# Kernel optimization log

Measured on AMD Instinct MI355X. Metric: run time of the kernel, lower is better.

Reference implementation:

```python
import jax, jax.numpy as jnp
import numpy as np

D_MODEL = 1024
HEADS = 16
D_K = D_MODEL // HEADS


def setup_inputs() -> dict:
    key = jax.random.key(0)
    ks = jax.random.split(key, 11)
    bs, seq = 2, 2048
    scale = 1.0 / np.sqrt(D_MODEL)
    inp = {
        "query": jax.random.normal(ks[0], (bs, seq, D_MODEL), jnp.float32),
        "key": jax.random.normal(ks[1], (bs, seq, D_MODEL), jnp.float32),
        "value": jax.random.normal(ks[2], (bs, seq, D_MODEL), jnp.float32),
        # nn.Linear weights: y = x @ W.T + b, W shape [out, in]
        "Wq": jax.random.normal(ks[3], (D_MODEL, D_MODEL), jnp.float32) * scale,
        "bq": jnp.zeros((D_MODEL,), jnp.float32),
        "Wk": jax.random.normal(ks[4], (D_MODEL, D_MODEL), jnp.float32) * scale,
        "bk": jnp.zeros((D_MODEL,), jnp.float32),
        "Wv": jax.random.normal(ks[5], (D_MODEL, D_MODEL), jnp.float32) * scale,
        "bv": jnp.zeros((D_MODEL,), jnp.float32),
        "Wo": jax.random.normal(ks[6], (D_MODEL, D_MODEL), jnp.float32) * scale,
        "bo": jnp.zeros((D_MODEL,), jnp.float32),
    }
    return inp


def _split_heads(x, bs):
    # [b, s, d_model] -> [b, h, s, d_k]
    return x.reshape(bs, -1, HEADS, D_K).transpose(0, 2, 1, 3)


def reference(query, key, value, Wq, bq, Wk, bk, Wv, bv, Wo, bo):
    bs = query.shape[0]
    q = _split_heads(query @ Wq.T + bq, bs)
    k = _split_heads(key @ Wk.T + bk, bs)
    v = _split_heads(value @ Wv.T + bv, bs)
    # scaled dot-product attention (dropout is identity at eval)
    logits = jnp.einsum("bhqd,bhkd->bhqk", q, k) / np.sqrt(D_K).astype(np.float32)
    probs = jax.nn.softmax(logits, axis=-1)
    scores = jnp.einsum("bhqk,bhkd->bhqd", probs, v)  # [b, h, s, d_k]
    concat = scores.transpose(0, 2, 1, 3).reshape(bs, -1, D_MODEL)
    output = concat @ Wo.T + bo
    return (output, scores)
```

## Files before the change

### kernel.cpp

```cpp
#include <hip/hip_runtime.h>
#include <stdint.h>
#include <math.h>

typedef __bf16 bf16;
typedef __bf16 bf16x4 __attribute__((ext_vector_type(4)));
typedef __bf16 bf16x8 __attribute__((ext_vector_type(8)));
typedef float floatx4 __attribute__((ext_vector_type(4)));
typedef float floatx16 __attribute__((ext_vector_type(16)));

#define CEXP 0.1803368801111204f

__global__ __launch_bounds__(256) void wcvt_kernel(
    const float* __restrict__ Wq, const float* __restrict__ Wk,
    const float* __restrict__ Wv, const float* __restrict__ Wo,
    bf16* __restrict__ dst)
{
  const float* src = (blockIdx.y == 0) ? Wq : (blockIdx.y == 1) ? Wk
                   : (blockIdx.y == 2) ? Wv : Wo;
  bf16* d = dst + (size_t)blockIdx.y * 1048576;
  const int i = (blockIdx.x * 256 + threadIdx.x) * 4;
  const floatx4 v = *(const floatx4*)(src + i);
  bf16x4 o;
#pragma unroll
  for (int j = 0; j < 4; ++j) o[j] = (bf16)v[j];
  *(bf16x4*)(d + i) = o;
}

__device__ __forceinline__ void gemm_body(
    const float* __restrict__ A, const bf16* __restrict__ Ab,
    const bf16* __restrict__ Wb, const float* __restrict__ bias,
    void* __restrict__ Cout, const int mode, const float oscale)
{
  __shared__ __align__(16) bf16 As[128 * 72];
  __shared__ __align__(16) bf16 Bs[128 * 72];
  const int tid  = threadIdx.x;
  const int wave = tid >> 6;
  const int lane = tid & 63;
  const int mlane = lane & 15;
  const int quad  = lane >> 4;
  const int m0 = blockIdx.x * 128;
  const int n0 = blockIdx.y * 128;
  const int wm = (wave >> 1) * 64;
  const int wn = (wave & 1) * 64;
  const int arow = tid >> 4, ac4 = (tid & 15) * 4;
  const int wrow = tid >> 3, wc8 = (tid & 7) * 8;

  floatx4 a_pf[8];
  bf16x8  ab_pf[4];
  bf16x8  w_pf[4];

  auto load_a = [&](int k0) {
    if (mode == 1) {
#pragma unroll
      for (int c = 0; c < 4; ++c) {
        const int token = m0 + c * 32 + wrow;
        const int b = token >> 11, s = token & 2047;
        const int h = k0 >> 6;
        ab_pf[c] = *(const bf16x8*)(Ab + (((size_t)(b * 16 + h) * 2048 + s) << 6) + wc8);
      }
    } else {
#pragma unroll
      for (int rr = 0; rr < 8; ++rr)
        a_pf[rr] = *(const floatx4*)(A + (size_t)(m0 + rr * 16 + arow) * 1024 + k0 + ac4);
    }
  };
  auto load_w = [&](int k0) {
#pragma unroll
    for (int c = 0; c < 4; ++c)
      w_pf[c] = *(const bf16x8*)(Wb + (size_t)(n0 + c * 32 + wrow) * 1024 + k0 + wc8);
  };

  load_a(0);
  load_w(0);

  floatx4 acc[4][4] = {};

  for (int k0 = 0; k0 < 1024; k0 += 64) {
    if (mode == 1) {
#pragma unroll
      for (int c = 0; c < 4; ++c)
        *(bf16x8*)&As[(c * 32 + wrow) * 72 + wc8] = ab_pf[c];
    } else {
#pragma unroll
      for (int rr = 0; rr < 8; ++rr) {
        bf16x4 ac;
#pragma unroll
        for (int j = 0; j < 4; ++j) ac[j] = (bf16)a_pf[rr][j];
        *(bf16x4*)&As[(rr * 16 + arow) * 72 + ac4] = ac;
      }
    }
#pragma unroll
    for (int c = 0; c < 4; ++c)
      *(bf16x8*)&Bs[(c * 32 + wrow) * 72 + wc8] = w_pf[c];
    __syncthreads();

    if (k0 + 64 < 1024) { load_a(k0 + 64); load_w(k0 + 64); }

#pragma unroll
    for (int kk = 0; kk < 64; kk += 32) {
      bf16x8 af[4], bfr[4];
#pragma unroll
      for (int t = 0; t < 4; ++t) {
        af[t]  = *(const bf16x8*)&As[(wm + t * 16 + mlane) * 72 + kk + quad * 8];
        bfr[t] = *(const bf16x8*)&Bs[(wn + t * 16 + mlane) * 72 + kk + quad * 8];
      }
#pragma unroll
      for (int mt = 0; mt < 4; ++mt)
#pragma unroll
        for (int nt = 0; nt < 4; ++nt)
          acc[mt][nt] = __builtin_amdgcn_mfma_f32_16x16x32_bf16(
              af[mt], bfr[nt], acc[mt][nt], 0, 0, 0);
    }
    __syncthreads();
  }

  if (mode == 2) {
    bf16* T = (wave < 2) ? &As[wave * 4608] : &Bs[(wave - 2) * 4608];
#pragma unroll
    for (int nt = 0; nt < 4; ++nt) {
      const float bv = bias[n0 + wn + nt * 16 + mlane];
#pragma unroll
      for (int mt = 0; mt < 4; ++mt) {
        bf16x4 t4;
#pragma unroll
        for (int r = 0; r < 4; ++r)
          t4[r] = (bf16)((acc[mt][nt][r] + bv) * oscale);
        *(bf16x4*)&T[(nt * 16 + mlane) * 72 + mt * 16 + quad * 4] = t4;
      }
    }
    asm volatile("s_waitcnt lgkmcnt(0)" ::: "memory");
    const int token0 = m0 + wm;
    const int bb = token0 >> 11;
    const int srow0 = token0 & 2047;
    const int h = (n0 + wn) >> 6;
    const int dl = lane >> 3;
    const int s8 = (lane & 7) * 8;
    bf16* outp = (bf16*)Cout + ((size_t)(bb * 16 + h) << 17);
#pragma unroll
    for (int p = 0; p < 8; ++p) {
      const int dk = p * 8 + dl;
      const bf16x8 v8 = *(const bf16x8*)&T[dk * 72 + s8];
      *(bf16x8*)&outp[((size_t)dk << 11) + srow0 + s8] = v8;
    }
    return;
  }

#pragma unroll
  for (int nt = 0; nt < 4; ++nt) {
    const int col = n0 + wn + nt * 16 + mlane;
    const float bv = bias[col];
#pragma unroll
    for (int mt = 0; mt < 4; ++mt) {
#pragma unroll
      for (int r = 0; r < 4; ++r) {
        const int row = m0 + wm + mt * 16 + quad * 4 + r;
        const float v = (acc[mt][nt][r] + bv) * oscale;
        if (mode == 0) {
          const int b = row >> 11, s = row & 2047;
          const int h = col >> 6, dk = col & 63;
          ((bf16*)Cout)[(((size_t)(b * 16 + h) * 2048 + s) << 6) + dk] = (bf16)v;
        } else {
          ((float*)Cout)[(size_t)row * 1024 + col] = v;
        }
      }
    }
  }
}

__global__ __launch_bounds__(256) void qkv_kernel(
    const float* __restrict__ q, const float* __restrict__ k, const float* __restrict__ v,
    const bf16* __restrict__ Wb,
    const float* __restrict__ bq, const float* __restrict__ bk, const float* __restrict__ bv,
    bf16* __restrict__ Qw, bf16* __restrict__ Kw, bf16* __restrict__ Vw)
{
  const int z = blockIdx.z;
  const float* A = (z == 0) ? q : (z == 1) ? k : v;
  const bf16* W  = Wb + (size_t)z * 1048576;
  const float* B = (z == 0) ? bq : (z == 1) ? bk : bv;
  if (z == 2)      gemm_body(A, nullptr, W, B, Vw, 2, 1.0f);
  else if (z == 1) gemm_body(A, nullptr, W, B, Kw, 0, 1.0f);
  else             gemm_body(A, nullptr, W, B, Qw, 0, CEXP);
}

__global__ __launch_bounds__(256) void out_kernel(
    const bf16* __restrict__ Sb, const bf16* __restrict__ Wob,
    const float* __restrict__ bo, float* __restrict__ out)
{
  gemm_body(nullptr, Sb, Wob, bo, out, 1, 1.0f);
}

__global__ __launch_bounds__(256, 2) void attn_kernel(
    const bf16* __restrict__ Qw, const bf16* __restrict__ Kw,
    const bf16* __restrict__ Vtg, float* __restrict__ scores,
    bf16* __restrict__ Sb)
{
  __shared__ __align__(16) char smem[2 * 2 * 64 * 136];

  const int tid  = threadIdx.x;
  const int wave = tid >> 6;
  const int lane = tid & 63;
  const int c    = lane & 31;
  const int hi   = lane >> 5;

  const int g = blockIdx.x + (blockIdx.y << 4);
  const int slot = g >> 3;
  const int bh = ((g & 7) << 2) + (slot >> 4);
  const int q0 = (slot & 15) << 7;
  const size_t base = (size_t)bh << 17;

  const int srow = tid >> 2;
  const int sce  = (tid & 3) * 16;

  bf16x8 qf[4];
#pragma unroll
  for (int m = 0; m < 4; ++m)
    qf[m] = *(const bf16x8*)
        &Qw[base + (size_t)(q0 + wave * 32 + c) * 64 + m * 16 + hi * 8];

  floatx16 o[2] = {};
  float rs = 0.f;

  bf16x8 kpf[2], vpf[2];
  auto load_kv = [&](int kt) {
    const bf16* kp = &Kw[base + (size_t)(kt + srow) * 64 + sce];
    kpf[0] = *(const bf16x8*)kp;
    kpf[1] = *(const bf16x8*)(kp + 8);
    const bf16* vp = &Vtg[base + (size_t)srow * 2048 + kt + sce];
    vpf[0] = *(const bf16x8*)vp;
    vpf[1] = *(const bf16x8*)(vp + 8);
  };
  auto stage = [&](int b) {
    char* kr = smem + b * 17408 + srow * 136 + (tid & 3) * 32;
    char* vr = kr + 8704;
    *(bf16x4*)(kr +  0) = ((const bf16x4*)&kpf[0])[0];
    *(bf16x4*)(kr +  8) = ((const bf16x4*)&kpf[0])[1];
    *(bf16x4*)(kr + 16) = ((const bf16x4*)&kpf[1])[0];
    *(bf16x4*)(kr + 24) = ((const bf16x4*)&kpf[1])[1];
    *(bf16x4*)(vr +  0) = ((const bf16x4*)&vpf[0])[0];
    *(bf16x4*)(vr +  8) = ((const bf16x4*)&vpf[0])[1];
    *(bf16x4*)(vr + 16) = ((const bf16x4*)&vpf[1])[0];
    *(bf16x4*)(vr + 24) = ((const bf16x4*)&vpf[1])[1];
  };

  load_kv(0);
  stage(0);
  load_kv(64);
  __syncthreads();

  for (int kt = 0; kt < 2048; kt += 64) {
    const int cur = (kt >> 6) & 1;
    if (kt + 64 < 2048) {
      stage(cur ^ 1);
      if (kt + 128 < 2048) load_kv(kt + 128);
    }
    const char* KsB = smem + cur * 17408;
    const char* VsB = KsB + 8704;

#pragma unroll
    for (int ks = 0; ks < 2; ++ks) {
      const char* krow = KsB + (ks * 32 + c) * 136;
      floatx16 s = {};
      __builtin_amdgcn_s_setprio(1);
#pragma unroll
      for (int m = 0; m < 4; ++m) {
        bf16x8 a;
        ((bf16x4*)&a)[0] = *(const bf16x4*)(krow + m * 32 + hi * 16);
        ((bf16x4*)&a)[1] = *(const bf16x4*)(krow + m * 32 + hi * 16 + 8);
        s = __builtin_amdgcn_mfma_f32_32x32x16_bf16(a, qf[m], s, 0, 0, 0);
      }
      __builtin_amdgcn_s_setprio(0);

      float p[16];
#pragma unroll
      for (int i = 0; i < 16; ++i) p[i] = __builtin_amdgcn_exp2f(s[i]);
#pragma unroll
      for (int i = 0; i < 16; ++i) rs += p[i];

      uint32_t ulo[4], uhi[4];
#pragma unroll
      for (int gg = 0; gg < 4; ++gg) {
        asm("v_cvt_pk_bf16_f32 %0, %1, %2"
            : "=v"(ulo[gg]) : "v"(p[4 * gg]), "v"(p[4 * gg + 1]));
        asm("v_cvt_pk_bf16_f32 %0, %1, %2"
            : "=v"(uhi[gg]) : "v"(p[4 * gg + 2]), "v"(p[4 * gg + 3]));
      }

      __builtin_amdgcn_s_setprio(1);
#pragma unroll
      for (int t = 0; t < 2; ++t) {
        uint32_t w0 = ulo[2 * t], w2 = ulo[2 * t + 1];
        uint32_t w1 = uhi[2 * t], w3 = uhi[2 * t + 1];
        asm("v_permlane32_swap_b32 %0, %1" : "+v"(w0), "+v"(w2));
        asm("v_permlane32_swap_b32 %0, %1" : "+v"(w1), "+v"(w3));
        union { bf16x8 v; uint32_t w[4]; } pu;
        pu.w[0] = w0; pu.w[1] = w1; pu.w[2] = w2; pu.w[3] = w3;
#pragma unroll
        for (int d = 0; d < 2; ++d) {
          const char* vrow = VsB + (d * 32 + c) * 136 + ks * 64 + t * 32 + hi * 16;
          bf16x8 va;
          ((bf16x4*)&va)[0] = *(const bf16x4*)(vrow);
          ((bf16x4*)&va)[1] = *(const bf16x4*)(vrow + 8);
          o[d] = __builtin_amdgcn_mfma_f32_32x32x16_bf16(va, pu.v, o[d], 0, 0, 0);
        }
      }
      __builtin_amdgcn_s_setprio(0);
    }
    __syncthreads();
  }

  rs += __shfl_xor(rs, 32, 64);
  const float inv = 1.0f / rs;

  const int q = q0 + wave * 32 + c;
  float* sr = scores + base + (size_t)q * 64;
  bf16*  br = Sb + base + (size_t)q * 64;
#pragma unroll
  for (int d = 0; d < 2; ++d)
#pragma unroll
    for (int gg = 0; gg < 4; ++gg) {
      const int dk = d * 32 + gg * 8 + hi * 4;
      floatx4 v4;
      bf16x4 b4;
#pragma unroll
      for (int i = 0; i < 4; ++i) {
        const float v = o[d][gg * 4 + i] * inv;
        v4[i] = v;
        b4[i] = (bf16)v;
      }
      *(floatx4*)(sr + dk) = v4;
      *(bf16x4*)(br + dk) = b4;
    }
}

extern "C" void kernel_launch(void* const* d_in, const int* in_sizes, int n_in,
                              void* d_out, int out_size, void* d_ws, size_t ws_size,
                              hipStream_t stream) {
  const float* query = (const float*)d_in[0];
  const float* key   = (const float*)d_in[1];
  const float* value = (const float*)d_in[2];
  const float* Wq = (const float*)d_in[3];
  const float* bq = (const float*)d_in[4];
  const float* Wk = (const float*)d_in[5];
  const float* bk = (const float*)d_in[6];
  const float* Wv = (const float*)d_in[7];
  const float* bv = (const float*)d_in[8];
  const float* Wo = (const float*)d_in[9];
  const float* bo = (const float*)d_in[10];

  float* out    = (float*)d_out;
  float* scores = out + (size_t)4194304;

  bf16* Wb  = (bf16*)d_ws;
  bf16* Qws = Wb + (size_t)4194304;
  bf16* Kws = Qws + (size_t)4194304;
  bf16* Vws = Kws + (size_t)4194304;
  bf16* Sb  = Vws + (size_t)4194304;

  wcvt_kernel<<<dim3(1024, 4), 256, 0, stream>>>(Wq, Wk, Wv, Wo, Wb);
  qkv_kernel<<<dim3(32, 8, 3), 256, 0, stream>>>(query, key, value, Wb,
                                                 bq, bk, bv, Qws, Kws, Vws);
  attn_kernel<<<dim3(16, 32), 256, 0, stream>>>(Qws, Kws, Vws, scores, Sb);
  out_kernel<<<dim3(32, 8), 256, 0, stream>>>(Sb, Wb + (size_t)3145728, bo, out);
}
```

Measured before the change: 228.4 us.

## Pre-convert activations to bf16 and stage GEMM tiles via global_load_lds

Adds a kernel that converts the fp32 query/key/value inputs to bf16, using the output buffer as scratch space. The GEMM body then stages A and W tiles straight from global memory into LDS with global_load_lds, which removes the register prefetch and the in-kernel conversion. LDS rows are now unpadded (stride 64), so the fragment reads may hit bank conflicts, and the register-level prefetch overlap across k-steps is gone: each step loads and then syncs. The separate conversion pass adds a full extra read and write of the activations.

```diff
diff --git a/kernel.cpp b/kernel.cpp
--- a/kernel.cpp
+++ b/kernel.cpp
@@ -9,6 +9,11 @@
 typedef float floatx16 __attribute__((ext_vector_type(16)));
 
 #define CEXP 0.1803368801111204f
+
+typedef __attribute__((address_space(1))) const void gvoid_t;
+typedef __attribute__((address_space(3))) void lvoid_t;
+#define GLOAD_LDS16(g, l) \
+  __builtin_amdgcn_global_load_lds((gvoid_t*)(g), (lvoid_t*)(l), 16, 0, 0)
 
 __global__ __launch_bounds__(256) void wcvt_kernel(
     const float* __restrict__ Wq, const float* __restrict__ Wk,
@@ -26,13 +31,28 @@
   *(bf16x4*)(d + i) = o;
 }
 
+__global__ __launch_bounds__(256) void xcvt_kernel(
+    const float* __restrict__ q, const float* __restrict__ k,
+    const float* __restrict__ v,
+    bf16* __restrict__ Qb, bf16* __restrict__ Kb, bf16* __restrict__ Vb)
+{
+  const float* src = (blockIdx.y == 0) ? q : (blockIdx.y == 1) ? k : v;
+  bf16* d = (blockIdx.y == 0) ? Qb : (blockIdx.y == 1) ? Kb : Vb;
+  const int i = (blockIdx.x * 256 + threadIdx.x) * 4;
+  const floatx4 val = *(const floatx4*)(src + i);
+  bf16x4 o;
+#pragma unroll
+  for (int j = 0; j < 4; ++j) o[j] = (bf16)val[j];
+  *(bf16x4*)(d + i) = o;
+}
+
 __device__ __forceinline__ void gemm_body(
-    const float* __restrict__ A, const bf16* __restrict__ Ab,
+    const bf16* __restrict__ Ab,
     const bf16* __restrict__ Wb, const float* __restrict__ bias,
     void* __restrict__ Cout, const int mode, const float oscale)
 {
-  __shared__ __align__(16) bf16 As[128 * 72];
-  __shared__ __align__(16) bf16 Bs[128 * 72];
+  __shared__ __align__(16) char smem[36864];
+
   const int tid  = threadIdx.x;
   const int wave = tid >> 6;
   const int lane = tid & 63;
@@ -42,67 +62,46 @@
   const int n0 = blockIdx.y * 128;
   const int wm = (wave >> 1) * 64;
   const int wn = (wave & 1) * 64;
-  const int arow = tid >> 4, ac4 = (tid & 15) * 4;
-  const int wrow = tid >> 3, wc8 = (tid & 7) * 8;
-
-  floatx4 a_pf[8];
-  bf16x8  ab_pf[4];
-  bf16x8  w_pf[4];
-
-  auto load_a = [&](int k0) {
-    if (mode == 1) {
-#pragma unroll
-      for (int c = 0; c < 4; ++c) {
-        const int token = m0 + c * 32 + wrow;
-        const int b = token >> 11, s = token & 2047;
+
+  const int srow8 = tid >> 3;
+  const int ch    = tid & 7;
+
+  auto stage = [&](int k0) {
+    bf16* Abuf = (bf16*)smem;
+    bf16* Bbuf = (bf16*)(smem + 16384);
+#pragma unroll
+    for (int i = 0; i < 4; ++i) {
+      const int row = i * 32 + srow8;
+      const bf16* ga;
+      if (mode == 1) {
+        const int token = m0 + row;
+        const int bb = token >> 11, s = token & 2047;
         const int h = k0 >> 6;
-        ab_pf[c] = *(const bf16x8*)(Ab + (((size_t)(b * 16 + h) * 2048 + s) << 6) + wc8);
-      }
-    } else {
-#pragma unroll
-      for (int rr = 0; rr < 8; ++rr)
-        a_pf[rr] = *(const floatx4*)(A + (size_t)(m0 + rr * 16 + arow) * 1024 + k0 + ac4);
+        ga = Ab + (((size_t)(bb * 16 + h) * 2048 + s) << 6) + ch * 8;
+      } else {
+        ga = Ab + (size_t)(m0 + row) * 1024 + k0 + ch * 8;
+      }
+      GLOAD_LDS16(ga, Abuf + i * 2048 + wave * 512);
+      const bf16* gb = Wb + (size_t)(n0 + row) * 1024 + k0 + ch * 8;
+      GLOAD_LDS16(gb, Bbuf + i * 2048 + wave * 512);
     }
   };
-  auto load_w = [&](int k0) {
-#pragma unroll
-    for (int c = 0; c < 4; ++c)
-      w_pf[c] = *(const bf16x8*)(Wb + (size_t)(n0 + c * 32 + wrow) * 1024 + k0 + wc8);
-  };
-
-  load_a(0);
-  load_w(0);
 
   floatx4 acc[4][4] = {};
 
   for (int k0 = 0; k0 < 1024; k0 += 64) {
-    if (mode == 1) {
-#pragma unroll
-      for (int c = 0; c < 4; ++c)
-        *(bf16x8*)&As[(c * 32 + wrow) * 72 + wc8] = ab_pf[c];
-    } else {
-#pragma unroll
-      for (int rr = 0; rr < 8; ++rr) {
-        bf16x4 ac;
-#pragma unroll
-        for (int j = 0; j < 4; ++j) ac[j] = (bf16)a_pf[rr][j];
-        *(bf16x4*)&As[(rr * 16 + arow) * 72 + ac4] = ac;
-      }
-    }
-#pragma unroll
-    for (int c = 0; c < 4; ++c)
-      *(bf16x8*)&Bs[(c * 32 + wrow) * 72 + wc8] = w_pf[c];
+    stage(k0);
     __syncthreads();
 
-    if (k0 + 64 < 1024) { load_a(k0 + 64); load_w(k0 + 64); }
-
+    const bf16* As = (const bf16*)smem;
+    const bf16* Bs = (const bf16*)(smem + 16384);
 #pragma unroll
     for (int kk = 0; kk < 64; kk += 32) {
       bf16x8 af[4], bfr[4];
 #pragma unroll
       for (int t = 0; t < 4; ++t) {
-        af[t]  = *(const bf16x8*)&As[(wm + t * 16 + mlane) * 72 + kk + quad * 8];
-        bfr[t] = *(const bf16x8*)&Bs[(wn + t * 16 + mlane) * 72 + kk + quad * 8];
+        af[t]  = *(const bf16x8*)&As[(wm + t * 16 + mlane) * 64 + kk + quad * 8];
+        bfr[t] = *(const bf16x8*)&Bs[(wn + t * 16 + mlane) * 64 + kk + quad * 8];
       }
 #pragma unroll
       for (int mt = 0; mt < 4; ++mt)
@@ -115,7 +114,7 @@
   }
 
   if (mode == 2) {
-    bf16* T = (wave < 2) ? &As[wave * 4608] : &Bs[(wave - 2) * 4608];
+    bf16* T = (bf16*)smem + wave * 4608;
 #pragma unroll
     for (int nt = 0; nt < 4; ++nt) {
       const float bv = bias[n0 + wn + nt * 16 + mlane];
@@ -168,25 +167,26 @@
 }
 
 __global__ __launch_bounds__(256) void qkv_kernel(
-    const float* __restrict__ q, const float* __restrict__ k, const float* __restrict__ v,
-    const bf16* __restrict__ Wb,
-    const float* __restrict__ bq, const float* __restrict__ bk, const float* __restrict__ bv,
+    const bf16* __restrict__ Qb, const bf16* __restrict__ Kb,
+    const bf16* __restrict__ Vb, const bf16* __restrict__ Wb,
+    const float* __restrict__ bq, const float* __restrict__ bk,
+    const float* __restrict__ bv,
     bf16* __restrict__ Qw, bf16* __restrict__ Kw, bf16* __restrict__ Vw)
 {
   const int z = blockIdx.z;
-  const float* A = (z == 0) ? q : (z == 1) ? k : v;
-  const bf16* W  = Wb + (size_t)z * 1048576;
+  const bf16* A = (z == 0) ? Qb : (z == 1) ? Kb : Vb;
+  const bf16* W = Wb + (size_t)z * 1048576;
   const float* B = (z == 0) ? bq : (z == 1) ? bk : bv;
-  if (z == 2)      gemm_body(A, nullptr, W, B, Vw, 2, 1.0f);
-  else if (z == 1) gemm_body(A, nullptr, W, B, Kw, 0, 1.0f);
-  else             gemm_body(A, nullptr, W, B, Qw, 0, CEXP);
+  if (z == 2)      gemm_body(A, W, B, Vw, 2, 1.0f);
+  else if (z == 1) gemm_body(A, W, B, Kw, 0, 1.0f);
+  else             gemm_body(A, W, B, Qw, 0, CEXP);
 }
 
 __global__ __launch_bounds__(256) void out_kernel(
     const bf16* __restrict__ Sb, const bf16* __restrict__ Wob,
     const float* __restrict__ bo, float* __restrict__ out)
 {
-  gemm_body(nullptr, Sb, Wob, bo, out, 1, 1.0f);
+  gemm_body(Sb, Wob, bo, out, 1, 1.0f);
 }
 
 __global__ __launch_bounds__(256, 2) void attn_kernel(
@@ -351,13 +351,18 @@
   float* scores = out + (size_t)4194304;
 
   bf16* Wb  = (bf16*)d_ws;
-  bf16* Qws = Wb + (size_t)4194304;
+  bf16* Qws = Wb  + (size_t)4194304;
   bf16* Kws = Qws + (size_t)4194304;
   bf16* Vws = Kws + (size_t)4194304;
   bf16* Sb  = Vws + (size_t)4194304;
 
+  bf16* Qb = (bf16*)out;
+  bf16* Kb = Qb + (size_t)4194304;
+  bf16* Vb = (bf16*)scores;
+
   wcvt_kernel<<<dim3(1024, 4), 256, 0, stream>>>(Wq, Wk, Wv, Wo, Wb);
-  qkv_kernel<<<dim3(32, 8, 3), 256, 0, stream>>>(query, key, value, Wb,
+  xcvt_kernel<<<dim3(4096, 3), 256, 0, stream>>>(query, key, value, Qb, Kb, Vb);
+  qkv_kernel<<<dim3(32, 8, 3), 256, 0, stream>>>(Qb, Kb, Vb, Wb,
                                                  bq, bk, bv, Qws, Kws, Vws);
   attn_kernel<<<dim3(16, 32), 256, 0, stream>>>(Qws, Kws, Vws, scores, Sb);
   out_kernel<<<dim3(32, 8), 256, 0, stream>>>(Sb, Wb + (size_t)3145728, bo, out);
```

Result: slower. 238.0 us (+4.2%).
